# Performance work log

Measured on AMD Instinct MI355X. Metric: run time of the kernel, lower is better.

The kernel has to match this reference:

```python
import jax, jax.numpy as jnp
import numpy as np

HDIM = 256
VOCAB = 100000
NUM_CLASSES = 5
N_LEAVES = 2048


def _build_tree(n_leaves):
    # balanced pairing tree; leaves are nodes [0, n_leaves), internal nodes appended
    # in topological order so every parent index > its children's indices.
    frontier = list(range(n_leaves)); nid = n_leaves; left = []; right = []
    while len(frontier) > 1:
        nxt = []
        for a, b in zip(frontier[0::2], frontier[1::2]):
            left.append(a); right.append(b); nxt.append(nid); nid += 1
        if len(frontier) % 2 == 1:
            nxt.append(frontier[-1])
        frontier = nxt
    return np.asarray(left, np.int64), np.asarray(right, np.int64)


def setup_inputs() -> dict:
    key = jax.random.key(0)
    ks = jax.random.split(key, 12)
    left, right = _build_tree(N_LEAVES)
    s = 1.0 / float(np.sqrt(HDIM))
    W = lambda k, shp: (jax.random.normal(k, shp, jnp.float32) * s)
    z = lambda n: jnp.zeros((n,), jnp.float32)
    return {
        "word_ids": jax.random.randint(ks[0], (N_LEAVES,), 0, VOCAB),
        "left_idx": jnp.asarray(left),
        "right_idx": jnp.asarray(right),
        "emb": jax.random.normal(ks[1], (VOCAB, HDIM), jnp.float32) * 0.1,
        "Wi": W(ks[2], (HDIM, HDIM)), "bi": z(HDIM),
        "Wo": W(ks[3], (HDIM, HDIM)), "bo": z(HDIM),
        "Wu": W(ks[4], (HDIM, HDIM)), "bu": z(HDIM),
        "Ui": W(ks[5], (HDIM, 2 * HDIM)), "bui": z(HDIM),
        "Uo": W(ks[6], (HDIM, 2 * HDIM)), "buo": z(HDIM),
        "Uu": W(ks[7], (HDIM, 2 * HDIM)), "buu": z(HDIM),
        "Uf1": W(ks[8], (HDIM, HDIM)), "bf1": z(HDIM),
        "Uf2": W(ks[9], (HDIM, HDIM)), "bf2": z(HDIM),
        "Wp": W(ks[10], (NUM_CLASSES, HDIM)), "bp": z(NUM_CLASSES),
    }


def reference(word_ids, left_idx, right_idx, emb,
              Wi, bi, Wo, bo, Wu, bu,
              Ui, bui, Uo, buo, Uu, buu,
              Uf1, bf1, Uf2, bf2, Wp, bp):
    sig = jax.nn.sigmoid
    relu = jax.nn.relu
    n_leaves = word_ids.shape[0]
    n_internal = left_idx.shape[0]
    n_nodes = n_leaves + n_internal

    # --- leaf nodes, fully vectorized ---
    e = emb[word_ids]                                  # [L, H]
    i = sig(e @ Wi.T + bi)
    o = sig(e @ Wo.T + bo)
    u = relu(e @ Wu.T + bu)
    c_leaf = i * u
    h_leaf = o * relu(c_leaf)

    h_buf = jnp.zeros((n_nodes, HDIM), e.dtype).at[:n_leaves].set(h_leaf)
    node_ids = jnp.arange(n_leaves, n_nodes)

    # --- internal nodes: sequential by topological order ---
    def step(hb, xs):
        l, r, idx = xs
        lh = hb[l]; rh = hb[r]                         # [H] each
        cat = jnp.concatenate([lh, rh])                # [2H]
        ii = sig(Ui @ cat + bui)
        oo = sig(Uo @ cat + buo)
        uu = relu(Uu @ cat + buu)
        # NOTE: faithful to source — forget gates multiply child h, not child c
        c = ii * uu + sig(Uf1 @ lh + bf1) * lh + sig(Uf2 @ rh + bf2) * rh
        h = oo * relu(c)
        return hb.at[idx].set(h), None

    h_buf, _ = jax.lax.scan(step, h_buf, (left_idx, right_idx, node_ids))

    # per-node class logits (original concatenates projection(h) across all nodes)
    logits = h_buf @ Wp.T + bp                         # [n_nodes, numClasses]
    return logits
```

## Files before the change

kernel.cpp:

```cpp
#include <hip/hip_runtime.h>
#include <math.h>

#define H 256

__device__ __forceinline__ float sigmoidf_(float x) {
    return 1.0f / (1.0f + __expf(-x));
}

__device__ __forceinline__ float dot4(float4 a, float4 b, float acc) {
    acc = fmaf(a.x, b.x, acc);
    acc = fmaf(a.y, b.y, acc);
    acc = fmaf(a.z, b.z, acc);
    acc = fmaf(a.w, b.w, acc);
    return acc;
}

__global__ __launch_bounds__(512, 4) void leaf_kernel(
    const int* __restrict__ word_ids, const float* __restrict__ emb,
    const float* __restrict__ Wi, const float* __restrict__ Wo, const float* __restrict__ Wu,
    const float* __restrict__ bi, const float* __restrict__ bo, const float* __restrict__ bu,
    float* __restrict__ h_buf, int n_leaves, int ncoh)
{
    const int tid = threadIdx.x;
    const int jb8 = blockIdx.x * 8;
    const int coh = blockIdx.y;
    const int kc  = tid & 63;
    const int jl  = tid >> 6;
    const int j   = jb8 + jl;

    __shared__ float s_e[4][H];

    const float4 wiv = *(const float4*)&Wi[(size_t)j * H + 4 * kc];
    const float4 wov = *(const float4*)&Wo[(size_t)j * H + 4 * kc];
    const float4 wuv = *(const float4*)&Wu[(size_t)j * H + 4 * kc];
    const float bij = bi[j], boj = bo[j], buj = bu[j];

    const int sl = tid >> 7;
    const int se = (tid & 127) * 2;

    const int nq = (n_leaves + 3) >> 2;

    float2 v = make_float2(0.f, 0.f);
    {
        int l = coh * 4 + sl;
        if (l < n_leaves) {
            int wid = word_ids[l];
            v = *(const float2*)&emb[(size_t)wid * H + se];
        }
    }
    for (int q = coh; q < nq; q += ncoh) {
        __syncthreads();
        *(float2*)&s_e[sl][se] = v;
        __syncthreads();
        int qn = q + ncoh;
        if (qn < nq) {
            int l = qn * 4 + sl;
            if (l < n_leaves) {
                int wid = word_ids[l];
                v = *(const float2*)&emb[(size_t)wid * H + se];
            }
        }
        float ai[4], ao[4], au[4];
#pragma unroll
        for (int lf = 0; lf < 4; ++lf) {
            float4 x = *(const float4*)&s_e[lf][4 * kc];
            ai[lf] = dot4(x, wiv, 0.f);
            ao[lf] = dot4(x, wov, 0.f);
            au[lf] = dot4(x, wuv, 0.f);
        }
#pragma unroll
        for (int m = 1; m <= 32; m <<= 1) {
#pragma unroll
            for (int lf = 0; lf < 4; ++lf) {
                ai[lf] += __shfl_xor(ai[lf], m);
                ao[lf] += __shfl_xor(ao[lf], m);
                au[lf] += __shfl_xor(au[lf], m);
            }
        }
        if (kc == 0) {
#pragma unroll
            for (int lf = 0; lf < 4; ++lf) {
                int l = q * 4 + lf;
                if (l < n_leaves) {
                    float ii = sigmoidf_(ai[lf] + bij);
                    float oo = sigmoidf_(ao[lf] + boj);
                    float uu = fmaxf(au[lf] + buj, 0.f);
                    float h  = oo * fmaxf(ii * uu, 0.f);
                    h_buf[(size_t)l * H + j] = h;
                }
            }
        }
    }
}

__global__ __launch_bounds__(512, 4) void level_kernel(
    const int* __restrict__ left_idx, const int* __restrict__ right_idx,
    const float* __restrict__ Ui, const float* __restrict__ Uo, const float* __restrict__ Uu,
    const float* __restrict__ Uf1, const float* __restrict__ Uf2,
    const float* __restrict__ bui, const float* __restrict__ buo, const float* __restrict__ buu,
    const float* __restrict__ bf1, const float* __restrict__ bf2,
    float* __restrict__ h_buf, int tbase, int lvl, int n_leaves, int ncoh)
{
    const int tid = threadIdx.x;
    const int jb8 = blockIdx.x * 8;
    const int coh = blockIdx.y;
    const int kc  = tid & 63;
    const int jl  = tid >> 6;
    const int j   = jb8 + jl;

    __shared__ float s_cat[2 * H];

    const float4 wi0 = *(const float4*)&Ui[(size_t)j * 2 * H + 4 * kc];
    const float4 wi1 = *(const float4*)&Ui[(size_t)j * 2 * H + H + 4 * kc];
    const float4 wo0 = *(const float4*)&Uo[(size_t)j * 2 * H + 4 * kc];
    const float4 wo1 = *(const float4*)&Uo[(size_t)j * 2 * H + H + 4 * kc];
    const float4 wu0 = *(const float4*)&Uu[(size_t)j * 2 * H + 4 * kc];
    const float4 wu1 = *(const float4*)&Uu[(size_t)j * 2 * H + H + 4 * kc];
    const float4 wf0 = *(const float4*)&Uf1[(size_t)j * H + 4 * kc];
    const float4 wf1 = *(const float4*)&Uf2[(size_t)j * H + 4 * kc];
    const float b_i = bui[j], b_o = buo[j], b_u = buu[j];
    const float b_1 = bf1[j], b_2 = bf2[j];

    float v = 0.f;
    if (coh < lvl) {
        int t  = tbase + coh;
        int lc = __builtin_amdgcn_readfirstlane(left_idx[t]);
        int rc = __builtin_amdgcn_readfirstlane(right_idx[t]);
        v = (tid < H) ? h_buf[(size_t)lc * H + tid]
                      : h_buf[(size_t)rc * H + (tid - H)];
    }
    for (int idx = coh; idx < lvl; idx += ncoh) {
        __syncthreads();
        s_cat[tid] = v;
        __syncthreads();
        int idxn = idx + ncoh;
        if (idxn < lvl) {
            int tn = tbase + idxn;
            int lc = __builtin_amdgcn_readfirstlane(left_idx[tn]);
            int rc = __builtin_amdgcn_readfirstlane(right_idx[tn]);
            v = (tid < H) ? h_buf[(size_t)lc * H + tid]
                          : h_buf[(size_t)rc * H + (tid - H)];
        }
        float4 x0 = *(const float4*)&s_cat[4 * kc];
        float4 x1 = *(const float4*)&s_cat[H + 4 * kc];
        float a_i = dot4(x0, wi0, 0.f); a_i = dot4(x1, wi1, a_i);
        float a_o = dot4(x0, wo0, 0.f); a_o = dot4(x1, wo1, a_o);
        float a_u = dot4(x0, wu0, 0.f); a_u = dot4(x1, wu1, a_u);
        float f1  = dot4(x0, wf0, 0.f);
        float f2  = dot4(x1, wf1, 0.f);
#pragma unroll
        for (int m = 1; m <= 32; m <<= 1) {
            a_i += __shfl_xor(a_i, m);
            a_o += __shfl_xor(a_o, m);
            a_u += __shfl_xor(a_u, m);
            f1  += __shfl_xor(f1,  m);
            f2  += __shfl_xor(f2,  m);
        }
        if (kc == 0) {
            float lh = s_cat[j];
            float rh = s_cat[H + j];
            float ii  = sigmoidf_(a_i + b_i);
            float oo  = sigmoidf_(a_o + b_o);
            float uu  = fmaxf(a_u + b_u, 0.f);
            float ff1 = sigmoidf_(f1 + b_1);
            float ff2 = sigmoidf_(f2 + b_2);
            float c   = ii * uu + ff1 * lh + ff2 * rh;
            float h   = oo * fmaxf(c, 0.f);
            h_buf[(size_t)(n_leaves + tbase + idx) * H + j] = h;
        }
    }
}

__global__ __launch_bounds__(256) void proj_kernel(
    const float* __restrict__ h_buf, const float* __restrict__ Wp,
    const float* __restrict__ bp, float* __restrict__ out, int total)
{
    int t = blockIdx.x * 256 + threadIdx.x;
    if (t >= total) return;
    int node = t / 5;
    int cls  = t - node * 5;
    const float4* hr = (const float4*)(h_buf + (size_t)node * H);
    const float4* wr = (const float4*)(Wp + (size_t)cls * H);
    float acc = 0.f;
#pragma unroll 8
    for (int k = 0; k < H / 4; ++k) {
        float4 a = hr[k], b = wr[k];
        acc += a.x * b.x + a.y * b.y + a.z * b.z + a.w * b.w;
    }
    out[t] = acc + bp[cls];
}

extern "C" void kernel_launch(void* const* d_in, const int* in_sizes, int n_in,
                              void* d_out, int out_size, void* d_ws, size_t ws_size,
                              hipStream_t stream)
{
    const int*   word_ids  = (const int*)  d_in[0];
    const int*   left_idx  = (const int*)  d_in[1];
    const int*   right_idx = (const int*)  d_in[2];
    const float* emb       = (const float*)d_in[3];
    const float* Wi  = (const float*)d_in[4];  const float* bi  = (const float*)d_in[5];
    const float* Wo  = (const float*)d_in[6];  const float* bo  = (const float*)d_in[7];
    const float* Wu  = (const float*)d_in[8];  const float* bu  = (const float*)d_in[9];
    const float* Ui  = (const float*)d_in[10]; const float* bui = (const float*)d_in[11];
    const float* Uo  = (const float*)d_in[12]; const float* buo = (const float*)d_in[13];
    const float* Uu  = (const float*)d_in[14]; const float* buu = (const float*)d_in[15];
    const float* Uf1 = (const float*)d_in[16]; const float* bf1 = (const float*)d_in[17];
    const float* Uf2 = (const float*)d_in[18]; const float* bf2 = (const float*)d_in[19];
    const float* Wp  = (const float*)d_in[20]; const float* bp  = (const float*)d_in[21];

    const int n_leaves   = in_sizes[0];
    const int n_internal = in_sizes[1];
    const int n_nodes    = n_leaves + n_internal;
    (void)n_in; (void)out_size; (void)ws_size;

    float* h_buf = (float*)d_ws;

    int nq = (n_leaves + 3) >> 2;
    int ncohL = nq < 32 ? nq : 32;
    leaf_kernel<<<dim3(32, ncohL), 512, 0, stream>>>(
        word_ids, emb, Wi, Wo, Wu, bi, bo, bu, h_buf, n_leaves, ncohL);

    int frontier = n_leaves;
    int tbase = 0;
    while (frontier > 1) {
        int lvl  = frontier >> 1;
        int ncoh = lvl < 32 ? lvl : 32;
        level_kernel<<<dim3(32, ncoh), 512, 0, stream>>>(
            left_idx, right_idx, Ui, Uo, Uu, Uf1, Uf2,
            bui, buo, buu, bf1, bf2, h_buf, tbase, lvl, n_leaves, ncoh);
        tbase += lvl;
        frontier = lvl + (frontier & 1);
    }

    int total = n_nodes * 5;
    proj_kernel<<<(total + 255) / 256, 256, 0, stream>>>(h_buf, Wp, bp, (float*)d_out, total);
}
```

Baseline: 357.1 us.

## Split each output row over 16 lanes with register inputs and DPP reductions

Leaf and level kernels now give each output row 16 lanes instead of a full 64-lane wavefront. Each lane keeps 16 or 32 weights in registers and loads its child or embedding slice straight from global memory into registers, so the shared-memory staging and the two __syncthreads per item are gone. The cross-lane sums use row_shl DPP adds in place of 64-wide shfl_xor trees, and the two forget-gate dot products share one DPP reduction that is split at the half row. Blocks shrink to 256 threads with up to 64 cohorts per level, which raises register pressure and makes 16 lanes issue redundant global loads of the same child rows.

```diff
diff --git a/kernel.cpp b/kernel.cpp
--- a/kernel.cpp
+++ b/kernel.cpp
@@ -15,85 +15,85 @@
     return acc;
 }
 
-__global__ __launch_bounds__(512, 4) void leaf_kernel(
+#define ROW_SHL1 0x101
+#define ROW_SHL2 0x102
+#define ROW_SHL4 0x104
+#define ROW_SHL8 0x108
+
+template<int CTRL>
+__device__ __forceinline__ float dpp_addf(float v) {
+    int s = __builtin_amdgcn_update_dpp(0, __float_as_int(v), CTRL, 0xF, 0xF, true);
+    return v + __int_as_float(s);
+}
+template<int CTRL>
+__device__ __forceinline__ float dpp_movf(float v) {
+    int s = __builtin_amdgcn_update_dpp(0, __float_as_int(v), CTRL, 0xF, 0xF, true);
+    return __int_as_float(s);
+}
+
+__global__ __launch_bounds__(256) void leaf_kernel(
     const int* __restrict__ word_ids, const float* __restrict__ emb,
     const float* __restrict__ Wi, const float* __restrict__ Wo, const float* __restrict__ Wu,
     const float* __restrict__ bi, const float* __restrict__ bo, const float* __restrict__ bu,
     float* __restrict__ h_buf, int n_leaves, int ncoh)
 {
-    const int tid = threadIdx.x;
-    const int jb8 = blockIdx.x * 8;
-    const int coh = blockIdx.y;
-    const int kc  = tid & 63;
-    const int jl  = tid >> 6;
-    const int j   = jb8 + jl;
-
-    __shared__ float s_e[4][H];
-
-    const float4 wiv = *(const float4*)&Wi[(size_t)j * H + 4 * kc];
-    const float4 wov = *(const float4*)&Wo[(size_t)j * H + 4 * kc];
-    const float4 wuv = *(const float4*)&Wu[(size_t)j * H + 4 * kc];
+    const int tid  = threadIdx.x;
+    const int lane = tid & 63;
+    const int wv   = tid >> 6;
+    const int ks   = lane & 15;
+    const int jl   = lane >> 4;
+    const int j    = blockIdx.x * 16 + wv * 4 + jl;
+    const int coh  = blockIdx.y;
+
+    float4 wi[4], wo[4], wu[4];
+    {
+        const float4* pi = (const float4*)(Wi + (size_t)j * H + ks * 16);
+        const float4* po = (const float4*)(Wo + (size_t)j * H + ks * 16);
+        const float4* pu = (const float4*)(Wu + (size_t)j * H + ks * 16);
+#pragma unroll
+        for (int c = 0; c < 4; ++c) { wi[c] = pi[c]; wo[c] = po[c]; wu[c] = pu[c]; }
+    }
     const float bij = bi[j], boj = bo[j], buj = bu[j];
 
-    const int sl = tid >> 7;
-    const int se = (tid & 127) * 2;
-
-    const int nq = (n_leaves + 3) >> 2;
-
-    float2 v = make_float2(0.f, 0.f);
-    {
-        int l = coh * 4 + sl;
-        if (l < n_leaves) {
-            int wid = word_ids[l];
-            v = *(const float2*)&emb[(size_t)wid * H + se];
-        }
-    }
-    for (int q = coh; q < nq; q += ncoh) {
-        __syncthreads();
-        *(float2*)&s_e[sl][se] = v;
-        __syncthreads();
-        int qn = q + ncoh;
-        if (qn < nq) {
-            int l = qn * 4 + sl;
-            if (l < n_leaves) {
-                int wid = word_ids[l];
-                v = *(const float2*)&emb[(size_t)wid * H + se];
-            }
-        }
-        float ai[4], ao[4], au[4];
-#pragma unroll
-        for (int lf = 0; lf < 4; ++lf) {
-            float4 x = *(const float4*)&s_e[lf][4 * kc];
-            ai[lf] = dot4(x, wiv, 0.f);
-            ao[lf] = dot4(x, wov, 0.f);
-            au[lf] = dot4(x, wuv, 0.f);
-        }
-#pragma unroll
-        for (int m = 1; m <= 32; m <<= 1) {
-#pragma unroll
-            for (int lf = 0; lf < 4; ++lf) {
-                ai[lf] += __shfl_xor(ai[lf], m);
-                ao[lf] += __shfl_xor(ao[lf], m);
-                au[lf] += __shfl_xor(au[lf], m);
-            }
-        }
-        if (kc == 0) {
-#pragma unroll
-            for (int lf = 0; lf < 4; ++lf) {
-                int l = q * 4 + lf;
-                if (l < n_leaves) {
-                    float ii = sigmoidf_(ai[lf] + bij);
-                    float oo = sigmoidf_(ao[lf] + boj);
-                    float uu = fmaxf(au[lf] + buj, 0.f);
-                    float h  = oo * fmaxf(ii * uu, 0.f);
-                    h_buf[(size_t)l * H + j] = h;
-                }
-            }
-        }
-    }
-}
-
-__global__ __launch_bounds__(512, 4) void level_kernel(
+    float4 px[4];
+    if (coh < n_leaves) {
+        int wid = word_ids[coh];
+        const float4* pe = (const float4*)(emb + (size_t)wid * H + ks * 16);
+#pragma unroll
+        for (int c = 0; c < 4; ++c) px[c] = pe[c];
+    }
+    for (int l = coh; l < n_leaves; l += ncoh) {
+        float ai = 0.f, ao = 0.f, au = 0.f;
+#pragma unroll
+        for (int c = 0; c < 4; ++c) {
+            ai = dot4(px[c], wi[c], ai);
+            ao = dot4(px[c], wo[c], ao);
+            au = dot4(px[c], wu[c], au);
+        }
+        int ln = l + ncoh;
+        if (ln < n_leaves) {
+            int wid = word_ids[ln];
+            const float4* pe = (const float4*)(emb + (size_t)wid * H + ks * 16);
+#pragma unroll
+            for (int c = 0; c < 4; ++c) px[c] = pe[c];
+        }
+        ai = dpp_addf<ROW_SHL8>(ai); ai = dpp_addf<ROW_SHL4>(ai);
+        ai = dpp_addf<ROW_SHL2>(ai); ai = dpp_addf<ROW_SHL1>(ai);
+        ao = dpp_addf<ROW_SHL8>(ao); ao = dpp_addf<ROW_SHL4>(ao);
+        ao = dpp_addf<ROW_SHL2>(ao); ao = dpp_addf<ROW_SHL1>(ao);
+        au = dpp_addf<ROW_SHL8>(au); au = dpp_addf<ROW_SHL4>(au);
+        au = dpp_addf<ROW_SHL2>(au); au = dpp_addf<ROW_SHL1>(au);
+        if (ks == 0) {
+            float iv = sigmoidf_(ai + bij);
+            float ov = sigmoidf_(ao + boj);
+            float uv = fmaxf(au + buj, 0.f);
+            float h  = ov * fmaxf(iv * uv, 0.f);
+            h_buf[(size_t)l * H + j] = h;
+        }
+    }
+}
+
+__global__ __launch_bounds__(256) void level_kernel(
     const int* __restrict__ left_idx, const int* __restrict__ right_idx,
     const float* __restrict__ Ui, const float* __restrict__ Uo, const float* __restrict__ Uu,
     const float* __restrict__ Uf1, const float* __restrict__ Uf2,
@@ -101,73 +101,90 @@
     const float* __restrict__ bf1, const float* __restrict__ bf2,
     float* __restrict__ h_buf, int tbase, int lvl, int n_leaves, int ncoh)
 {
-    const int tid = threadIdx.x;
-    const int jb8 = blockIdx.x * 8;
-    const int coh = blockIdx.y;
-    const int kc  = tid & 63;
-    const int jl  = tid >> 6;
-    const int j   = jb8 + jl;
-
-    __shared__ float s_cat[2 * H];
-
-    const float4 wi0 = *(const float4*)&Ui[(size_t)j * 2 * H + 4 * kc];
-    const float4 wi1 = *(const float4*)&Ui[(size_t)j * 2 * H + H + 4 * kc];
-    const float4 wo0 = *(const float4*)&Uo[(size_t)j * 2 * H + 4 * kc];
-    const float4 wo1 = *(const float4*)&Uo[(size_t)j * 2 * H + H + 4 * kc];
-    const float4 wu0 = *(const float4*)&Uu[(size_t)j * 2 * H + 4 * kc];
-    const float4 wu1 = *(const float4*)&Uu[(size_t)j * 2 * H + H + 4 * kc];
-    const float4 wf0 = *(const float4*)&Uf1[(size_t)j * H + 4 * kc];
-    const float4 wf1 = *(const float4*)&Uf2[(size_t)j * H + 4 * kc];
+    const int tid  = threadIdx.x;
+    const int lane = tid & 63;
+    const int wv   = tid >> 6;
+    const int ks   = lane & 15;
+    const int jl   = lane >> 4;
+    const int j    = blockIdx.x * 16 + wv * 4 + jl;
+    const int coh  = blockIdx.y;
+
+    float4 wi[8], wo[8], wu[8], wf[8];
+    {
+        const float4* pi = (const float4*)(Ui + (size_t)j * 2 * H + ks * 32);
+        const float4* po = (const float4*)(Uo + (size_t)j * 2 * H + ks * 32);
+        const float4* pu = (const float4*)(Uu + (size_t)j * 2 * H + ks * 32);
+        const float*  fr = (ks < 8) ? (Uf1 + (size_t)j * H + ks * 32)
+                                    : (Uf2 + (size_t)j * H + (ks - 8) * 32);
+        const float4* pf = (const float4*)fr;
+#pragma unroll
+        for (int c = 0; c < 8; ++c) { wi[c]=pi[c]; wo[c]=po[c]; wu[c]=pu[c]; wf[c]=pf[c]; }
+    }
     const float b_i = bui[j], b_o = buo[j], b_u = buu[j];
     const float b_1 = bf1[j], b_2 = bf2[j];
 
-    float v = 0.f;
+    float4 px[8];
+    float  plh = 0.f, prh = 0.f;
+    int lc2 = 0, rc2 = 0;
     if (coh < lvl) {
-        int t  = tbase + coh;
-        int lc = __builtin_amdgcn_readfirstlane(left_idx[t]);
-        int rc = __builtin_amdgcn_readfirstlane(right_idx[t]);
-        v = (tid < H) ? h_buf[(size_t)lc * H + tid]
-                      : h_buf[(size_t)rc * H + (tid - H)];
-    }
+        int lc = left_idx[tbase + coh];
+        int rc = right_idx[tbase + coh];
+        const float4* xb = (const float4*)((ks < 8)
+            ? h_buf + (size_t)lc * H + ks * 32
+            : h_buf + (size_t)rc * H + (ks - 8) * 32);
+#pragma unroll
+        for (int c = 0; c < 8; ++c) px[c] = xb[c];
+        if (ks == 0) {
+            plh = h_buf[(size_t)lc * H + j];
+            prh = h_buf[(size_t)rc * H + j];
+        }
+        int i2 = coh + ncoh;
+        if (i2 < lvl) { lc2 = left_idx[tbase + i2]; rc2 = right_idx[tbase + i2]; }
+    }
+
     for (int idx = coh; idx < lvl; idx += ncoh) {
-        __syncthreads();
-        s_cat[tid] = v;
-        __syncthreads();
+        float lh = plh, rh = prh;
+        float ai = 0.f, ao = 0.f, au = 0.f, af = 0.f;
+#pragma unroll
+        for (int c = 0; c < 8; ++c) {
+            ai = dot4(px[c], wi[c], ai);
+            ao = dot4(px[c], wo[c], ao);
+            au = dot4(px[c], wu[c], au);
+            af = dot4(px[c], wf[c], af);
+        }
         int idxn = idx + ncoh;
         if (idxn < lvl) {
-            int tn = tbase + idxn;
-            int lc = __builtin_amdgcn_readfirstlane(left_idx[tn]);
-            int rc = __builtin_amdgcn_readfirstlane(right_idx[tn]);
-            v = (tid < H) ? h_buf[(size_t)lc * H + tid]
-                          : h_buf[(size_t)rc * H + (tid - H)];
-        }
-        float4 x0 = *(const float4*)&s_cat[4 * kc];
-        float4 x1 = *(const float4*)&s_cat[H + 4 * kc];
-        float a_i = dot4(x0, wi0, 0.f); a_i = dot4(x1, wi1, a_i);
-        float a_o = dot4(x0, wo0, 0.f); a_o = dot4(x1, wo1, a_o);
-        float a_u = dot4(x0, wu0, 0.f); a_u = dot4(x1, wu1, a_u);
-        float f1  = dot4(x0, wf0, 0.f);
-        float f2  = dot4(x1, wf1, 0.f);
-#pragma unroll
-        for (int m = 1; m <= 32; m <<= 1) {
-            a_i += __shfl_xor(a_i, m);
-            a_o += __shfl_xor(a_o, m);
-            a_u += __shfl_xor(a_u, m);
-            f1  += __shfl_xor(f1,  m);
-            f2  += __shfl_xor(f2,  m);
-        }
-        if (kc == 0) {
-            float lh = s_cat[j];
-            float rh = s_cat[H + j];
-            float ii  = sigmoidf_(a_i + b_i);
-            float oo  = sigmoidf_(a_o + b_o);
-            float uu  = fmaxf(a_u + b_u, 0.f);
-            float ff1 = sigmoidf_(f1 + b_1);
-            float ff2 = sigmoidf_(f2 + b_2);
-            float c   = ii * uu + ff1 * lh + ff2 * rh;
-            float h   = oo * fmaxf(c, 0.f);
+            const float4* xb = (const float4*)((ks < 8)
+                ? h_buf + (size_t)lc2 * H + ks * 32
+                : h_buf + (size_t)rc2 * H + (ks - 8) * 32);
+#pragma unroll
+            for (int c = 0; c < 8; ++c) px[c] = xb[c];
+            if (ks == 0) {
+                plh = h_buf[(size_t)lc2 * H + j];
+                prh = h_buf[(size_t)rc2 * H + j];
+            }
+            int idx2 = idxn + ncoh;
+            if (idx2 < lvl) { lc2 = left_idx[tbase + idx2]; rc2 = right_idx[tbase + idx2]; }
+        }
+        ai = dpp_addf<ROW_SHL8>(ai); ai = dpp_addf<ROW_SHL4>(ai);
+        ai = dpp_addf<ROW_SHL2>(ai); ai = dpp_addf<ROW_SHL1>(ai);
+        ao = dpp_addf<ROW_SHL8>(ao); ao = dpp_addf<ROW_SHL4>(ao);
+        ao = dpp_addf<ROW_SHL2>(ao); ao = dpp_addf<ROW_SHL1>(ao);
+        au = dpp_addf<ROW_SHL8>(au); au = dpp_addf<ROW_SHL4>(au);
+        au = dpp_addf<ROW_SHL2>(au); au = dpp_addf<ROW_SHL1>(au);
+        af = dpp_addf<ROW_SHL4>(af); af = dpp_addf<ROW_SHL2>(af);
+        af = dpp_addf<ROW_SHL1>(af);
+        float f2s = dpp_movf<ROW_SHL8>(af);
+
+        float iv  = sigmoidf_(ai + b_i);
+        float ov  = sigmoidf_(ao + b_o);
+        float uv  = fmaxf(au + b_u, 0.f);
+        float f1v = sigmoidf_(af + b_1);
+        float f2v = sigmoidf_(f2s + b_2);
+        float cc  = iv * uv + f1v * lh + f2v * rh;
+        float h   = ov * fmaxf(cc, 0.f);
+        if (ks == 0)
             h_buf[(size_t)(n_leaves + tbase + idx) * H + j] = h;
-        }
     }
 }
 
@@ -215,17 +232,16 @@
 
     float* h_buf = (float*)d_ws;
 
-    int nq = (n_leaves + 3) >> 2;
-    int ncohL = nq < 32 ? nq : 32;
-    leaf_kernel<<<dim3(32, ncohL), 512, 0, stream>>>(
+    int ncohL = n_leaves < 64 ? n_leaves : 64;
+    leaf_kernel<<<dim3(16, ncohL), 256, 0, stream>>>(
         word_ids, emb, Wi, Wo, Wu, bi, bo, bu, h_buf, n_leaves, ncohL);
 
     int frontier = n_leaves;
     int tbase = 0;
     while (frontier > 1) {
         int lvl  = frontier >> 1;
-        int ncoh = lvl < 32 ? lvl : 32;
-        level_kernel<<<dim3(32, ncoh), 512, 0, stream>>>(
+        int ncoh = lvl < 64 ? lvl : 64;
+        level_kernel<<<dim3(16, ncoh), 256, 0, stream>>>(
             left_idx, right_idx, Ui, Uo, Uu, Uf1, Uf2,
             bui, buo, buu, bf1, bf2, h_buf, tbase, lvl, n_leaves, ncoh);
         tbase += lvl;
```

Result: faster. 314.1 us (-12.1%).
